# Performance work log

Measured on AMD Instinct MI355X. Metric: run time of the kernel, lower is better.

The kernel has to match this reference:

```python
import jax, jax.numpy as jnp
import numpy as np

N_NODES = 50000
N_EDGES = 300000
IN_FEATS = 1433
HIDDEN = 16
OUT_FEATS = 7


def setup_inputs() -> dict:
    key = jax.random.key(0)
    k1, k2, k3, k4, k5, k6, k7, k8 = jax.random.split(key, 8)
    features = jax.random.normal(k1, (N_NODES, IN_FEATS), dtype=jnp.float32)
    src = jax.random.randint(k2, (N_EDGES,), 0, N_NODES, dtype=jnp.int32)
    dst = jax.random.randint(k3, (N_EDGES,), 0, N_NODES, dtype=jnp.int32)
    # Linear layer params (PyTorch default-ish init scale)
    s1 = 1.0 / np.sqrt(IN_FEATS)
    s2 = 1.0 / np.sqrt(HIDDEN)
    W1 = jax.random.uniform(k4, (IN_FEATS, HIDDEN), jnp.float32, -s1, s1)
    b1 = jax.random.uniform(k5, (HIDDEN,), jnp.float32, -s1, s1)
    W2 = jax.random.uniform(k6, (HIDDEN, OUT_FEATS), jnp.float32, -s2, s2)
    b2 = jax.random.uniform(k7, (OUT_FEATS,), jnp.float32, -s2, s2)
    return {"features": features, "src": src, "dst": dst,
            "W1": W1, "b1": b1, "W2": W2, "b2": b2}


def _gcn_layer(h, src, dst, W, b):
    # copy_src message + sum reduce + self term: h'_v = sum_{u->v} h_u + h_v
    agg = jax.ops.segment_sum(h[src], dst, num_segments=N_NODES) + h
    return agg @ W + b


def reference(features, src, dst, W1, b1, W2, b2):
    x = jax.nn.relu(_gcn_layer(features, src, dst, W1, b1))
    # dropout is identity in eval mode
    x = _gcn_layer(x, src, dst, W2, b2)
    return x
```

## Files before the change

kernel.cpp:

```cpp
#include <hip/hip_runtime.h>
#include <hip/hip_bf16.h>

#define N_NODES  50000
#define N_EDGES  300000
#define IN_FEATS 1433
#define HIDDEN   16
#define OUT_F    7
#define KPAD     1472
#define WROW     9

__device__ __forceinline__ unsigned short f2bf(float f) {
    unsigned int x = __float_as_uint(f);
    unsigned int r = x + 0x7fffu + ((x >> 16) & 1u);
    return (unsigned short)(r >> 16);
}

__global__ __launch_bounds__(256) void k1_gemm(
    const float* __restrict__ F, const float* __restrict__ W1,
    const float* __restrict__ b1, float* __restrict__ H,
    float* __restrict__ aggbuf)
{
    __shared__ unsigned int Wl[KPAD * WROW];
    const int tid = threadIdx.x;

    for (int idx = tid; idx < KPAD * 8; idx += 256) {
        int k = idx >> 3, c = idx & 7;
        unsigned int u = 0u;
        if (k < IN_FEATS) {
            unsigned int lo = f2bf(W1[k * 16 + 2 * c]);
            unsigned int hi = f2bf(W1[k * 16 + 2 * c + 1]);
            u = lo | (hi << 16);
        }
        Wl[k * WROW + c] = u;
    }
    __syncthreads();

    const int lane = tid & 63;
    const float b1v = b1[lane & 15];
    const int gwave  = blockIdx.x * 4 + (tid >> 6);
    const int nwaves = gridDim.x * 4;

    for (int ch = gwave; ch < N_NODES / 4; ch += nwaves) {
        const int r0 = ch * 4;
        const float* fp = F + (size_t)r0 * IN_FEATS;

        float v[64];
        #pragma unroll
        for (int i = 0; i < 64; ++i) v[i] = 0.f;

        #pragma unroll 2
        for (int i = 0; i < 22; ++i) {
            const int k = i * 64 + lane;
            const float f0 = fp[k];
            const float f1 = fp[IN_FEATS + k];
            const float f2 = fp[2 * IN_FEATS + k];
            const float f3 = fp[3 * IN_FEATS + k];
            float wv[16];
            #pragma unroll
            for (int c = 0; c < 8; ++c) {
                unsigned int u = Wl[k * WROW + c];
                wv[2 * c]     = __uint_as_float(u << 16);
                wv[2 * c + 1] = __uint_as_float(u & 0xffff0000u);
            }
            #pragma unroll
            for (int j = 0; j < 16; ++j) {
                v[j]      += f0 * wv[j];
                v[16 + j] += f1 * wv[j];
                v[32 + j] += f2 * wv[j];
                v[48 + j] += f3 * wv[j];
            }
        }
        {
            const int k = 1408 + lane;
            float f0 = 0.f, f1 = 0.f, f2 = 0.f, f3 = 0.f;
            if (k < IN_FEATS) {
                f0 = fp[k];
                f1 = fp[IN_FEATS + k];
                f2 = fp[2 * IN_FEATS + k];
                f3 = fp[3 * IN_FEATS + k];
            }
            float wv[16];
            #pragma unroll
            for (int c = 0; c < 8; ++c) {
                unsigned int u = Wl[k * WROW + c];
                wv[2 * c]     = __uint_as_float(u << 16);
                wv[2 * c + 1] = __uint_as_float(u & 0xffff0000u);
            }
            #pragma unroll
            for (int j = 0; j < 16; ++j) {
                v[j]      += f0 * wv[j];
                v[16 + j] += f1 * wv[j];
                v[32 + j] += f2 * wv[j];
                v[48 + j] += f3 * wv[j];
            }
        }

        #pragma unroll
        for (int d = 5; d >= 0; --d) {
            const int half = 1 << d;
            const bool hi = (lane >> d) & 1;
            #pragma unroll
            for (int t = 0; t < (1 << d); ++t) {
                float sent = hi ? v[t] : v[t + half];
                float recv = __shfl_xor(sent, half, 64);
                float keep = hi ? v[t + half] : v[t];
                v[t] = keep + recv;
            }
        }
        const size_t off = (size_t)r0 * 16 + lane;
        H[off] = v[0];
        aggbuf[off] = v[0] + b1v;
    }
}

__global__ __launch_bounds__(256) void k2_scatter1(
    const int* __restrict__ src, const int* __restrict__ dst,
    const float* __restrict__ H, float* __restrict__ aggbuf)
{
    int t = blockIdx.x * 256 + threadIdx.x;
    int e = t >> 4, j = t & 15;
    if (e < N_EDGES) {
        int s = src[e], d = dst[e];
        atomicAdd(&aggbuf[(size_t)d * 16 + j], H[(size_t)s * 16 + j]);
    }
}

__global__ __launch_bounds__(256) void k3_layer2(
    const float* __restrict__ aggbuf, const float* __restrict__ W2,
    const float* __restrict__ b2, float* __restrict__ G,
    float* __restrict__ out)
{
    int n = blockIdx.x * 256 + threadIdx.x;
    if (n >= N_NODES) return;
    const float* a = aggbuf + (size_t)n * 16;
    float x[16];
    #pragma unroll
    for (int k = 0; k < 16; ++k) { float vv = a[k]; x[k] = vv > 0.f ? vv : 0.f; }
    #pragma unroll
    for (int j = 0; j < OUT_F; ++j) {
        float g = 0.f;
        #pragma unroll
        for (int k = 0; k < 16; ++k) g += x[k] * W2[k * OUT_F + j];
        G[(size_t)n * OUT_F + j] = g;
        out[(size_t)n * OUT_F + j] = g + b2[j];
    }
}

__global__ __launch_bounds__(256) void k4_scatter2(
    const int* __restrict__ src, const int* __restrict__ dst,
    const float* __restrict__ G, float* __restrict__ out)
{
    int t = blockIdx.x * 256 + threadIdx.x;
    int e = t / OUT_F, j = t % OUT_F;
    if (e < N_EDGES) {
        atomicAdd(&out[(size_t)dst[e] * OUT_F + j], G[(size_t)src[e] * OUT_F + j]);
    }
}

extern "C" void kernel_launch(void* const* d_in, const int* in_sizes, int n_in,
                              void* d_out, int out_size, void* d_ws, size_t ws_size,
                              hipStream_t stream)
{
    const float* F  = (const float*)d_in[0];
    const int*   src = (const int*)d_in[1];
    const int*   dst = (const int*)d_in[2];
    const float* W1 = (const float*)d_in[3];
    const float* b1 = (const float*)d_in[4];
    const float* W2 = (const float*)d_in[5];
    const float* b2 = (const float*)d_in[6];
    float* out = (float*)d_out;

    float* H      = (float*)d_ws;
    float* aggbuf = H + (size_t)N_NODES * HIDDEN;
    float* G      = H;

    k1_gemm<<<768, 256, 0, stream>>>(F, W1, b1, H, aggbuf);
    k2_scatter1<<<(N_EDGES * 16) / 256, 256, 0, stream>>>(src, dst, H, aggbuf);
    k3_layer2<<<(N_NODES + 255) / 256, 256, 0, stream>>>(aggbuf, W2, b2, G, out);
    k4_scatter2<<<(N_EDGES * OUT_F + 255) / 256, 256, 0, stream>>>(src, dst, G, out);
}
```

Measured before the change: 118.7 us.

## Fuse four GCN kernels into one persistent kernel with grid barriers

Merges the layer-1 GEMM, both edge scatters and the layer-2 transform into a single persistent kernel of 512 blocks. The stages are separated by atomic-counter grid barriers, and the counter is zeroed with a memset before each launch. This removes the inter-kernel launch gaps and drains, at the cost of barrier spin time and a smaller grid for the GEMM stage. It depends on all 512 blocks being co-resident, which the 53KB of LDS per block and the 2-blocks-per-CU launch bound must allow.

Result: slower. 421.2 us (+254.7%).

```diff
diff --git a/kernel.cpp b/kernel.cpp
--- a/kernel.cpp
+++ b/kernel.cpp
@@ -8,6 +8,7 @@
 #define OUT_F    7
 #define KPAD     1472
 #define WROW     9
+#define GRID     512
 
 __device__ __forceinline__ unsigned short f2bf(float f) {
     unsigned int x = __float_as_uint(f);
@@ -15,10 +16,26 @@
     return (unsigned short)(r >> 16);
 }
 
-__global__ __launch_bounds__(256) void k1_gemm(
-    const float* __restrict__ F, const float* __restrict__ W1,
-    const float* __restrict__ b1, float* __restrict__ H,
-    float* __restrict__ aggbuf)
+__device__ __forceinline__ void grid_barrier(unsigned int* bar, unsigned int target) {
+    __syncthreads();
+    if (threadIdx.x == 0) {
+        __threadfence();
+        __hip_atomic_fetch_add(bar, 1u, __ATOMIC_ACQ_REL, __HIP_MEMORY_SCOPE_AGENT);
+        while (__hip_atomic_load(bar, __ATOMIC_ACQUIRE, __HIP_MEMORY_SCOPE_AGENT) < target) {
+            __builtin_amdgcn_s_sleep(8);
+        }
+    }
+    __syncthreads();
+    __threadfence();
+}
+
+__global__ __launch_bounds__(256, 2) void gcn_fused(
+    const float* __restrict__ F, const int* __restrict__ src,
+    const int* __restrict__ dst, const float* __restrict__ W1,
+    const float* __restrict__ b1, const float* __restrict__ W2,
+    const float* __restrict__ b2, float* __restrict__ H,
+    float* __restrict__ aggbuf, float* __restrict__ out,
+    unsigned int* __restrict__ bar)
 {
     __shared__ unsigned int Wl[KPAD * WROW];
     const int tid = threadIdx.x;
@@ -38,7 +55,7 @@
     const int lane = tid & 63;
     const float b1v = b1[lane & 15];
     const int gwave  = blockIdx.x * 4 + (tid >> 6);
-    const int nwaves = gridDim.x * 4;
+    const int nwaves = GRID * 4;
 
     for (int ch = gwave; ch < N_NODES / 4; ch += nwaves) {
         const int r0 = ch * 4;
@@ -111,48 +128,39 @@
         H[off] = v[0];
         aggbuf[off] = v[0] + b1v;
     }
-}
 
-__global__ __launch_bounds__(256) void k2_scatter1(
-    const int* __restrict__ src, const int* __restrict__ dst,
-    const float* __restrict__ H, float* __restrict__ aggbuf)
-{
-    int t = blockIdx.x * 256 + threadIdx.x;
-    int e = t >> 4, j = t & 15;
-    if (e < N_EDGES) {
+    grid_barrier(bar, GRID);
+
+    const int tglob = blockIdx.x * 256 + tid;
+    const int T = GRID * 256;
+    for (int i = tglob; i < N_EDGES * 16; i += T) {
+        int e = i >> 4, j = i & 15;
         int s = src[e], d = dst[e];
         atomicAdd(&aggbuf[(size_t)d * 16 + j], H[(size_t)s * 16 + j]);
     }
-}
 
-__global__ __launch_bounds__(256) void k3_layer2(
-    const float* __restrict__ aggbuf, const float* __restrict__ W2,
-    const float* __restrict__ b2, float* __restrict__ G,
-    float* __restrict__ out)
-{
-    int n = blockIdx.x * 256 + threadIdx.x;
-    if (n >= N_NODES) return;
-    const float* a = aggbuf + (size_t)n * 16;
-    float x[16];
-    #pragma unroll
-    for (int k = 0; k < 16; ++k) { float vv = a[k]; x[k] = vv > 0.f ? vv : 0.f; }
-    #pragma unroll
-    for (int j = 0; j < OUT_F; ++j) {
-        float g = 0.f;
+    grid_barrier(bar, 2 * GRID);
+
+    float* G = H;
+    for (int n = tglob; n < N_NODES; n += T) {
+        const float* a = aggbuf + (size_t)n * 16;
+        float x[16];
         #pragma unroll
-        for (int k = 0; k < 16; ++k) g += x[k] * W2[k * OUT_F + j];
-        G[(size_t)n * OUT_F + j] = g;
-        out[(size_t)n * OUT_F + j] = g + b2[j];
+        for (int k = 0; k < 16; ++k) { float vv = a[k]; x[k] = vv > 0.f ? vv : 0.f; }
+        #pragma unroll
+        for (int j = 0; j < OUT_F; ++j) {
+            float g = 0.f;
+            #pragma unroll
+            for (int k = 0; k < 16; ++k) g += x[k] * W2[k * OUT_F + j];
+            G[(size_t)n * OUT_F + j] = g;
+            out[(size_t)n * OUT_F + j] = g + b2[j];
+        }
     }
-}
 
-__global__ __launch_bounds__(256) void k4_scatter2(
-    const int* __restrict__ src, const int* __restrict__ dst,
-    const float* __restrict__ G, float* __restrict__ out)
-{
-    int t = blockIdx.x * 256 + threadIdx.x;
-    int e = t / OUT_F, j = t % OUT_F;
-    if (e < N_EDGES) {
+    grid_barrier(bar, 3 * GRID);
+
+    for (int i = tglob; i < N_EDGES * OUT_F; i += T) {
+        int e = i / OUT_F, j = i % OUT_F;
         atomicAdd(&out[(size_t)dst[e] * OUT_F + j], G[(size_t)src[e] * OUT_F + j]);
     }
 }
@@ -161,21 +169,21 @@
                               void* d_out, int out_size, void* d_ws, size_t ws_size,
                               hipStream_t stream)
 {
-    const float* F  = (const float*)d_in[0];
+    const float* F   = (const float*)d_in[0];
     const int*   src = (const int*)d_in[1];
     const int*   dst = (const int*)d_in[2];
-    const float* W1 = (const float*)d_in[3];
-    const float* b1 = (const float*)d_in[4];
-    const float* W2 = (const float*)d_in[5];
-    const float* b2 = (const float*)d_in[6];
+    const float* W1  = (const float*)d_in[3];
+    const float* b1  = (const float*)d_in[4];
+    const float* W2  = (const float*)d_in[5];
+    const float* b2  = (const float*)d_in[6];
     float* out = (float*)d_out;
 
     float* H      = (float*)d_ws;
     float* aggbuf = H + (size_t)N_NODES * HIDDEN;
-    float* G      = H;
+    unsigned int* bar = (unsigned int*)(aggbuf + (size_t)N_NODES * HIDDEN);
 
-    k1_gemm<<<768, 256, 0, stream>>>(F, W1, b1, H, aggbuf);
-    k2_scatter1<<<(N_EDGES * 16) / 256, 256, 0, stream>>>(src, dst, H, aggbuf);
-    k3_layer2<<<(N_NODES + 255) / 256, 256, 0, stream>>>(aggbuf, W2, b2, G, out);
-    k4_scatter2<<<(N_EDGES * OUT_F + 255) / 256, 256, 0, stream>>>(src, dst, G, out);
+    hipMemsetAsync(bar, 0, sizeof(unsigned int), stream);
+
+    gcn_fused<<<GRID, 256, 0, stream>>>(F, src, dst, W1, b1, W2, b2,
+                                        H, aggbuf, out, bar);
 }
```

## Build CSR by destination and replace atomic edge scatters with pull aggregation

Applied to the files above, without the earlier changes.

Builds a destination-sorted CSR each call using a histogram, a single-block scan and an atomic fill. The two edge-parallel atomicAdd scatter kernels are replaced with one-wave-per-node pull kernels that sum neighbour rows and reduce with shuffles, removing float atomics on the feature buffers. In exchange it adds a memset and three preprocessing launches, including a serial single-block scan, plus wasted lanes for nodes with few neighbours.

After: 267.7 us. 2.25x slower.

```diff
diff --git a/kernel.cpp b/kernel.cpp
--- a/kernel.cpp
+++ b/kernel.cpp
@@ -13,6 +13,55 @@
     unsigned int x = __float_as_uint(f);
     unsigned int r = x + 0x7fffu + ((x >> 16) & 1u);
     return (unsigned short)(r >> 16);
+}
+
+__global__ __launch_bounds__(256) void k_hist(const int* __restrict__ dst,
+                                              int* __restrict__ counts) {
+    int e = blockIdx.x * 256 + threadIdx.x;
+    if (e < N_EDGES) atomicAdd(&counts[dst[e]], 1);
+}
+
+__global__ __launch_bounds__(1024) void k_scan(const int* __restrict__ counts,
+                                               int* __restrict__ offsets,
+                                               int* __restrict__ cursor) {
+    __shared__ int L[1024];
+    const int t = threadIdx.x;
+    const int base = t * 49;
+    int sum = 0;
+    for (int i = 0; i < 49; ++i) {
+        int g = base + i;
+        if (g < N_NODES) sum += counts[g];
+    }
+    L[t] = sum;
+    __syncthreads();
+    for (int s = 1; s < 1024; s <<= 1) {
+        int v = (t >= s) ? L[t - s] : 0;
+        __syncthreads();
+        L[t] += v;
+        __syncthreads();
+    }
+    int run = L[t] - sum;
+    for (int i = 0; i < 49; ++i) {
+        int g = base + i;
+        if (g < N_NODES) {
+            int c = counts[g];
+            offsets[g] = run;
+            cursor[g]  = run;
+            run += c;
+        }
+    }
+    if (t == 1023) offsets[N_NODES] = L[1023];
+}
+
+__global__ __launch_bounds__(256) void k_fill(const int* __restrict__ src,
+                                              const int* __restrict__ dst,
+                                              int* __restrict__ cursor,
+                                              int* __restrict__ csr) {
+    int e = blockIdx.x * 256 + threadIdx.x;
+    if (e < N_EDGES) {
+        int pos = atomicAdd(&cursor[dst[e]], 1);
+        csr[pos] = src[e];
+    }
 }
 
 __global__ __launch_bounds__(256) void k1_gemm(
@@ -113,16 +162,27 @@
     }
 }
 
-__global__ __launch_bounds__(256) void k2_scatter1(
-    const int* __restrict__ src, const int* __restrict__ dst,
+__global__ __launch_bounds__(256) void k2_pull(
+    const int* __restrict__ offsets, const int* __restrict__ csr,
     const float* __restrict__ H, float* __restrict__ aggbuf)
 {
-    int t = blockIdx.x * 256 + threadIdx.x;
-    int e = t >> 4, j = t & 15;
-    if (e < N_EDGES) {
-        int s = src[e], d = dst[e];
-        atomicAdd(&aggbuf[(size_t)d * 16 + j], H[(size_t)s * 16 + j]);
-    }
+    const int v = blockIdx.x * 4 + (threadIdx.x >> 6);
+    if (v >= N_NODES) return;
+    const int lane = threadIdx.x & 63;
+    const int j = lane & 15, c = lane >> 4;
+    const int off = offsets[v], end = offsets[v + 1];
+    if (end <= off) return;
+    float acc = 0.f;
+    for (int base = off; base < end; base += 4) {
+        int idx = base + c;
+        if (idx < end) {
+            int s = csr[idx];
+            acc += H[(size_t)s * 16 + j];
+        }
+    }
+    acc += __shfl_xor(acc, 16, 64);
+    acc += __shfl_xor(acc, 32, 64);
+    if (lane < 16) aggbuf[(size_t)v * 16 + j] += acc;
 }
 
 __global__ __launch_bounds__(256) void k3_layer2(
@@ -146,36 +206,57 @@
     }
 }
 
-__global__ __launch_bounds__(256) void k4_scatter2(
-    const int* __restrict__ src, const int* __restrict__ dst,
+__global__ __launch_bounds__(256) void k4_pull(
+    const int* __restrict__ offsets, const int* __restrict__ csr,
     const float* __restrict__ G, float* __restrict__ out)
 {
-    int t = blockIdx.x * 256 + threadIdx.x;
-    int e = t / OUT_F, j = t % OUT_F;
-    if (e < N_EDGES) {
-        atomicAdd(&out[(size_t)dst[e] * OUT_F + j], G[(size_t)src[e] * OUT_F + j]);
-    }
+    const int v = blockIdx.x * 4 + (threadIdx.x >> 6);
+    if (v >= N_NODES) return;
+    const int lane = threadIdx.x & 63;
+    const int j = lane & 7, c = lane >> 3;
+    const int off = offsets[v], end = offsets[v + 1];
+    if (end <= off) return;
+    float acc = 0.f;
+    for (int base = off; base < end; base += 8) {
+        int idx = base + c;
+        if (idx < end && j < 7) {
+            acc += G[(size_t)csr[idx] * 7 + j];
+        }
+    }
+    acc += __shfl_xor(acc, 8, 64);
+    acc += __shfl_xor(acc, 16, 64);
+    acc += __shfl_xor(acc, 32, 64);
+    if (lane < 8 && j < 7) out[(size_t)v * 7 + j] += acc;
 }
 
 extern "C" void kernel_launch(void* const* d_in, const int* in_sizes, int n_in,
                               void* d_out, int out_size, void* d_ws, size_t ws_size,
                               hipStream_t stream)
 {
-    const float* F  = (const float*)d_in[0];
+    const float* F   = (const float*)d_in[0];
     const int*   src = (const int*)d_in[1];
     const int*   dst = (const int*)d_in[2];
-    const float* W1 = (const float*)d_in[3];
-    const float* b1 = (const float*)d_in[4];
-    const float* W2 = (const float*)d_in[5];
-    const float* b2 = (const float*)d_in[6];
+    const float* W1  = (const float*)d_in[3];
+    const float* b1  = (const float*)d_in[4];
+    const float* W2  = (const float*)d_in[5];
+    const float* b2  = (const float*)d_in[6];
     float* out = (float*)d_out;
 
     float* H      = (float*)d_ws;
     float* aggbuf = H + (size_t)N_NODES * HIDDEN;
     float* G      = H;
+    int* counts   = (int*)(aggbuf + (size_t)N_NODES * HIDDEN);
+    int* offsets  = counts + N_NODES;
+    int* cursor   = offsets + N_NODES + 1;
+    int* csr      = cursor + N_NODES;
+
+    hipMemsetAsync(counts, 0, N_NODES * sizeof(int), stream);
+    k_hist<<<(N_EDGES + 255) / 256, 256, 0, stream>>>(dst, counts);
+    k_scan<<<1, 1024, 0, stream>>>(counts, offsets, cursor);
+    k_fill<<<(N_EDGES + 255) / 256, 256, 0, stream>>>(src, dst, cursor, csr);
 
     k1_gemm<<<768, 256, 0, stream>>>(F, W1, b1, H, aggbuf);
-    k2_scatter1<<<(N_EDGES * 16) / 256, 256, 0, stream>>>(src, dst, H, aggbuf);
+    k2_pull<<<(N_NODES + 3) / 4, 256, 0, stream>>>(offsets, csr, H, aggbuf);
     k3_layer2<<<(N_NODES + 255) / 256, 256, 0, stream>>>(aggbuf, W2, b2, G, out);
-    k4_scatter2<<<(N_EDGES * OUT_F + 255) / 256, 256, 0, stream>>>(src, dst, G, out);
-}
+    k4_pull<<<(N_NODES + 3) / 4, 256, 0, stream>>>(offsets, csr, G, out);
+}
```
